# Performance work log

Hardware: AMD Instinct MI355X
Metric: run time of the kernel (lower is better)

## Reference

```python
import jax, jax.numpy as jnp
import numpy as np

H = 32        # num_attention_heads
KVH = 8       # num_key_value_heads
D = 2048      # hidden_size
HD = D // H   # head_dim = 64
GROUPS = H // KVH


def setup_inputs() -> dict:
    key = jax.random.key(0)
    k1, k2, k3, k4 = jax.random.split(key, 4)
    B, T = 2, 2048
    x = jax.random.normal(k1, (B, T, D), dtype=jnp.float32)
    wq = jax.random.normal(k2, (D, H * HD), dtype=jnp.float32) * (D ** -0.5)
    wkv = jax.random.normal(k3, (D, 2 * KVH * HD), dtype=jnp.float32) * (D ** -0.5)
    wo = jax.random.normal(k4, (H * HD, D), dtype=jnp.float32) * (D ** -0.5)
    return {"x": x, "wq": wq, "wkv": wkv, "wo": wo}


def reference(x, wq, wkv, wo):
    B, T, _ = x.shape
    scale = HD ** -0.5
    # projections
    q = (x @ wq).reshape(B, T, H, HD).transpose(0, 2, 1, 3)        # [B,H,T,hd]
    kv = x @ wkv                                                    # [B,T,2*KVH*hd]
    k, v = jnp.split(kv, 2, axis=-1)
    k = k.reshape(B, T, KVH, HD).transpose(0, 2, 1, 3)              # [B,KVH,T,hd]
    v = v.reshape(B, T, KVH, HD).transpose(0, 2, 1, 3)
    # repeat_interleave KV heads to match Q heads
    k = jnp.repeat(k, GROUPS, axis=1)                               # [B,H,T,hd]
    v = jnp.repeat(v, GROUPS, axis=1)
    scores = jnp.einsum('bhqd,bhkd->bhqk', q, k) * scale            # [B,H,T,T]
    causal = jnp.triu(jnp.ones((T, T), dtype=bool), k=1)
    scores = jnp.where(causal, -jnp.inf, scores)
    attn = jax.nn.softmax(scores, axis=-1)
    out = jnp.einsum('bhqk,bhkd->bhqd', attn, v)                    # [B,H,T,hd]
    out = out.transpose(0, 2, 1, 3).reshape(B, T, H * HD)
    return out @ wo
```

## Files before the change

### kernel.cpp

```cpp
#include <hip/hip_runtime.h>

using bf16   = __bf16;
using bf16x8 = __attribute__((ext_vector_type(8))) __bf16;
using f32x4  = __attribute__((ext_vector_type(4))) float;
using u32x4  = __attribute__((ext_vector_type(4))) unsigned;

#define T_SEQ 2048
#define NQKV 3072

__device__ __forceinline__ void async_cp16(const bf16* g, bf16* l) {
  __builtin_amdgcn_global_load_lds((__attribute__((address_space(1))) void*)(void*)g,
                                   (__attribute__((address_space(3))) void*)l, 16, 0, 0);
}

__global__ __launch_bounds__(256) void cvt_kernel(const float* __restrict__ in,
                                                  bf16* __restrict__ out) {
  long i = ((long)blockIdx.x * 256 + threadIdx.x) * 8;
  float4 a = *(const float4*)(in + i);
  float4 c = *(const float4*)(in + i + 4);
  bf16x8 v;
  v[0] = (bf16)a.x; v[1] = (bf16)a.y; v[2] = (bf16)a.z; v[3] = (bf16)a.w;
  v[4] = (bf16)c.x; v[5] = (bf16)c.y; v[6] = (bf16)c.z; v[7] = (bf16)c.w;
  *(bf16x8*)(out + i) = v;
}

__global__ __launch_bounds__(256) void transpose_cvt(const float* __restrict__ in,
                                                     bf16* __restrict__ out,
                                                     int R, int C) {
  __shared__ float tile[32][33];
  const int tc = blockIdx.x * 32;
  const int tr = blockIdx.y * 32;
  const int t = threadIdx.x;
  const int lr = t >> 5;
  const int lc = t & 31;
#pragma unroll
  for (int i = 0; i < 4; ++i)
    tile[lr + i * 8][lc] = in[(size_t)(tr + lr + i * 8) * C + tc + lc];
  __syncthreads();
#pragma unroll
  for (int i = 0; i < 4; ++i)
    out[(size_t)(tc + lr + i * 8) * R + tr + lc] = (bf16)tile[lc][lr + i * 8];
}

__global__ __launch_bounds__(256) void transpose_v(const bf16* __restrict__ in,
                                                   bf16* __restrict__ out) {
  __shared__ bf16 tile[32][33];
  const int c0 = blockIdx.x * 32;
  const int r0 = blockIdx.y * 32;
  const int t = threadIdx.x;
  const int lr = t >> 5;
  const int lc = t & 31;
#pragma unroll
  for (int i = 0; i < 4; ++i)
    tile[lr + i * 8][lc] = in[(size_t)(r0 + lr + i * 8) * NQKV + 2560 + c0 + lc];
  __syncthreads();
#pragma unroll
  for (int i = 0; i < 4; ++i) {
    int c = c0 + lr + i * 8;
    int r = r0 + lc;
    out[(size_t)((r >> 11) * 512 + c) * 2048 + (r & 2047)] = tile[lc][lr + i * 8];
  }
}

template <int KDIM, int BN, bool OUT_BF16>
__global__ __launch_bounds__(512, 2)
void gemm8_kernel(const bf16* __restrict__ A, const bf16* __restrict__ Bt,
                  void* __restrict__ Cout, int Ndim) {
  constexpr int NTILES = KDIM / 64;
  constexpr int NFR = BN / 64;
  __shared__ __attribute__((aligned(16))) bf16 As[2][256 * 64];
  __shared__ __attribute__((aligned(16))) bf16 Bs[2][BN * 64];

  const int tid  = threadIdx.x;
  const int lane = tid & 63;
  const int wave = tid >> 6;
  const int l16  = lane & 15;
  const int q4   = lane >> 4;
  const int wm   = (wave >> 2) * 128;
  const int wn   = (wave & 3) * (BN / 4);

  const long m0 = (long)blockIdx.y * 256;
  const long n0 = (long)blockIdx.x * BN;
  const bf16* Ag = A + m0 * (long)KDIM;
  const bf16* Bg = Bt + n0 * (long)KDIM;

  f32x4 acc[8][NFR] = {};

  auto stage = [&](int buf, int kt) {
    const long k0 = (long)kt * 64;
#pragma unroll
    for (int rr = 0; rr < 4; ++rr) {
      int ci = rr * 512 + tid;
      int row = ci >> 3;
      int ch = (ci & 7) ^ (row & 7);
      async_cp16(Ag + (long)row * KDIM + k0 + ch * 8, &As[buf][ci * 8]);
    }
#pragma unroll
    for (int rr = 0; rr < BN / 64; ++rr) {
      int ci = rr * 512 + tid;
      int row = ci >> 3;
      int ch = (ci & 7) ^ (row & 7);
      async_cp16(Bg + (long)row * KDIM + k0 + ch * 8, &Bs[buf][ci * 8]);
    }
  };

  stage(0, 0);
  stage(1, 1);

  for (int t = 0; t < NTILES; ++t) {
    const int cur = t & 1;
    if (t < NTILES - 1) {
      if constexpr (BN == 256) asm volatile("s_waitcnt vmcnt(8)" ::: "memory");
      else                     asm volatile("s_waitcnt vmcnt(6)" ::: "memory");
    } else {
      asm volatile("s_waitcnt vmcnt(0)" ::: "memory");
    }
    __builtin_amdgcn_s_barrier();

    bf16x8 a0[4], b0[NFR];
#pragma unroll
    for (int mt = 0; mt < 4; ++mt) {
      int row = wm + mt * 16 + l16;
      int slot = q4 ^ (row & 7);
      a0[mt] = *(const bf16x8*)&As[cur][row * 64 + slot * 8];
    }
#pragma unroll
    for (int nt = 0; nt < NFR; ++nt) {
      int row = wn + nt * 16 + l16;
      int slot = q4 ^ (row & 7);
      b0[nt] = *(const bf16x8*)&Bs[cur][row * 64 + slot * 8];
    }
    __builtin_amdgcn_s_setprio(1);
#pragma unroll
    for (int mt = 0; mt < 4; ++mt)
#pragma unroll
      for (int nt = 0; nt < NFR; ++nt)
        acc[mt][nt] = __builtin_amdgcn_mfma_f32_16x16x32_bf16(a0[mt], b0[nt],
                                                              acc[mt][nt], 0, 0, 0);
    __builtin_amdgcn_s_setprio(0);
    bf16x8 a0h[4];
#pragma unroll
    for (int mt = 0; mt < 4; ++mt) {
      int row = wm + 64 + mt * 16 + l16;
      int slot = q4 ^ (row & 7);
      a0h[mt] = *(const bf16x8*)&As[cur][row * 64 + slot * 8];
    }
    __builtin_amdgcn_s_setprio(1);
#pragma unroll
    for (int mt = 0; mt < 4; ++mt)
#pragma unroll
      for (int nt = 0; nt < NFR; ++nt)
        acc[4 + mt][nt] = __builtin_amdgcn_mfma_f32_16x16x32_bf16(a0h[mt], b0[nt],
                                                                  acc[4 + mt][nt], 0, 0, 0);
    __builtin_amdgcn_s_setprio(0);

    bf16x8 a1[4], a1h[4], b1[NFR];
#pragma unroll
    for (int mt = 0; mt < 4; ++mt) {
      int row = wm + mt * 16 + l16;
      int slot = (4 + q4) ^ (row & 7);
      a1[mt] = *(const bf16x8*)&As[cur][row * 64 + slot * 8];
    }
#pragma unroll
    for (int mt = 0; mt < 4; ++mt) {
      int row = wm + 64 + mt * 16 + l16;
      int slot = (4 + q4) ^ (row & 7);
      a1h[mt] = *(const bf16x8*)&As[cur][row * 64 + slot * 8];
    }
#pragma unroll
    for (int nt = 0; nt < NFR; ++nt) {
      int row = wn + nt * 16 + l16;
      int slot = (4 + q4) ^ (row & 7);
      b1[nt] = *(const bf16x8*)&Bs[cur][row * 64 + slot * 8];
    }
    asm volatile("s_waitcnt lgkmcnt(0)" ::: "memory");
    __builtin_amdgcn_sched_barrier(0);
    __builtin_amdgcn_s_barrier();
    if (t + 2 < NTILES) stage(cur, t + 2);

    __builtin_amdgcn_s_setprio(1);
#pragma unroll
    for (int mt = 0; mt < 4; ++mt)
#pragma unroll
      for (int nt = 0; nt < NFR; ++nt)
        acc[mt][nt] = __builtin_amdgcn_mfma_f32_16x16x32_bf16(a1[mt], b1[nt],
                                                              acc[mt][nt], 0, 0, 0);
#pragma unroll
    for (int mt = 0; mt < 4; ++mt)
#pragma unroll
      for (int nt = 0; nt < NFR; ++nt)
        acc[4 + mt][nt] = __builtin_amdgcn_mfma_f32_16x16x32_bf16(a1h[mt], b1[nt],
                                                                  acc[4 + mt][nt], 0, 0, 0);
    __builtin_amdgcn_s_setprio(0);
  }

#pragma unroll
  for (int mt = 0; mt < 8; ++mt)
#pragma unroll
    for (int nt = 0; nt < NFR; ++nt)
#pragma unroll
      for (int r = 0; r < 4; ++r) {
        long row = m0 + wm + mt * 16 + q4 * 4 + r;
        long col = n0 + wn + nt * 16 + l16;
        float v = acc[mt][nt][r];
        if constexpr (OUT_BF16)
          ((bf16*)Cout)[row * Ndim + col] = (bf16)v;
        else
          ((float*)Cout)[row * Ndim + col] = v;
      }
}

__global__ __launch_bounds__(256, 3)
void attn_kernel(const bf16* __restrict__ qkv, const bf16* __restrict__ vT,
                 bf16* __restrict__ outb) {
  __shared__ __attribute__((aligned(16))) bf16 Ks[64 * 64];
  __shared__ __attribute__((aligned(16))) bf16 Vs[64 * 64];

  const int tid  = threadIdx.x;
  const int lane = tid & 63;
  const int wave = tid >> 6;
  const int l16  = lane & 15;
  const int q4   = lane >> 4;

  const int bid = blockIdx.x;
  const int qt  = 15 - (bid >> 6);
  const int bh  = bid & 63;
  const int b   = bh >> 5;
  const int h   = bh & 31;
  const int kvh = h >> 2;
  const long rowbase = (long)b * T_SEQ;

  const int qrow0 = qt * 128;
  const int wq0   = qrow0 + wave * 32;
  const float cexp = 0.125f * 1.4426950408889634f;

  bf16x8 aq[2][2];
#pragma unroll
  for (int mt = 0; mt < 2; ++mt)
#pragma unroll
    for (int ks = 0; ks < 2; ++ks) {
      bf16x8 v = *(const bf16x8*)(qkv +
          (rowbase + wq0 + mt * 16 + l16) * (long)NQKV + h * 64 + ks * 32 + q4 * 8);
#pragma unroll
      for (int i = 0; i < 8; ++i) v[i] = (bf16)((float)v[i] * cexp);
      aq[mt][ks] = v;
    }

  bf16x8 ones_f;
#pragma unroll
  for (int i = 0; i < 8; ++i) ones_f[i] = (l16 == 0) ? (bf16)1.0f : (bf16)0.0f;

  f32x4 o[2][4] = {};
  f32x4 o_l[2] = {};

  const bf16* kbase = qkv + rowbase * (long)NQKV + 2048 + kvh * 64;
  const bf16* vbase = vT + ((long)b * 512 + kvh * 64) * 2048;

  for (int j0 = 0; j0 < qrow0 + 128; j0 += 64) {
    __syncthreads();
    {
#pragma unroll
      for (int h2 = 0; h2 < 2; ++h2) {
        int ci  = h2 * 256 + tid;
        int row = ci >> 3;
        int ch  = (ci & 7) ^ (row & 7);
        *(bf16x8*)&Ks[ci * 8] =
            *(const bf16x8*)(kbase + (long)(j0 + row) * NQKV + ch * 8);
        *(bf16x8*)&Vs[ci * 8] =
            *(const bf16x8*)(vbase + (long)row * 2048 + j0 + ch * 8);
      }
    }
    __syncthreads();
    if (j0 > wq0 + 31) continue;

    f32x4 s[2][4] = {};
#pragma unroll
    for (int ks = 0; ks < 2; ++ks) {
      bf16x8 bk[4];
#pragma unroll
      for (int nt = 0; nt < 4; ++nt) {
        int row  = nt * 16 + l16;
        int slot = (ks * 4 + q4) ^ (row & 7);
        bk[nt] = *(const bf16x8*)&Ks[row * 64 + slot * 8];
      }
#pragma unroll
      for (int mt = 0; mt < 2; ++mt)
#pragma unroll
        for (int nt = 0; nt < 4; ++nt)
          s[mt][nt] = __builtin_amdgcn_mfma_f32_16x16x32_bf16(bk[nt], aq[mt][ks],
                                                              s[mt][nt], 0, 0, 0);
    }

    if (j0 + 63 > wq0) {
#pragma unroll
      for (int mt = 0; mt < 2; ++mt)
#pragma unroll
        for (int nt = 0; nt < 4; ++nt)
#pragma unroll
          for (int r = 0; r < 4; ++r) {
            int rg = wq0 + mt * 16 + l16;
            int cg = j0 + nt * 16 + q4 * 4 + r;
            if (cg > rg) s[mt][nt][r] = -__builtin_inff();
          }
    }

    bf16x8 ap[2][2];
#pragma unroll
    for (int mt = 0; mt < 2; ++mt) {
      unsigned pk0, pk1, pk2, pk3, pk4, pk5, pk6, pk7;
      {
        float p0 = __builtin_amdgcn_exp2f(s[mt][0][0]);
        float p1 = __builtin_amdgcn_exp2f(s[mt][0][1]);
        float p2 = __builtin_amdgcn_exp2f(s[mt][0][2]);
        float p3 = __builtin_amdgcn_exp2f(s[mt][0][3]);
        asm("v_cvt_pk_bf16_f32 %0, %1, %2" : "=v"(pk0) : "v"(p0), "v"(p1));
        asm("v_cvt_pk_bf16_f32 %0, %1, %2" : "=v"(pk1) : "v"(p2), "v"(p3));
      }
      {
        float p0 = __builtin_amdgcn_exp2f(s[mt][1][0]);
        float p1 = __builtin_amdgcn_exp2f(s[mt][1][1]);
        float p2 = __builtin_amdgcn_exp2f(s[mt][1][2]);
        float p3 = __builtin_amdgcn_exp2f(s[mt][1][3]);
        asm("v_cvt_pk_bf16_f32 %0, %1, %2" : "=v"(pk2) : "v"(p0), "v"(p1));
        asm("v_cvt_pk_bf16_f32 %0, %1, %2" : "=v"(pk3) : "v"(p2), "v"(p3));
      }
      {
        float p0 = __builtin_amdgcn_exp2f(s[mt][2][0]);
        float p1 = __builtin_amdgcn_exp2f(s[mt][2][1]);
        float p2 = __builtin_amdgcn_exp2f(s[mt][2][2]);
        float p3 = __builtin_amdgcn_exp2f(s[mt][2][3]);
        asm("v_cvt_pk_bf16_f32 %0, %1, %2" : "=v"(pk4) : "v"(p0), "v"(p1));
        asm("v_cvt_pk_bf16_f32 %0, %1, %2" : "=v"(pk5) : "v"(p2), "v"(p3));
      }
      {
        float p0 = __builtin_amdgcn_exp2f(s[mt][3][0]);
        float p1 = __builtin_amdgcn_exp2f(s[mt][3][1]);
        float p2 = __builtin_amdgcn_exp2f(s[mt][3][2]);
        float p3 = __builtin_amdgcn_exp2f(s[mt][3][3]);
        asm("v_cvt_pk_bf16_f32 %0, %1, %2" : "=v"(pk6) : "v"(p0), "v"(p1));
        asm("v_cvt_pk_bf16_f32 %0, %1, %2" : "=v"(pk7) : "v"(p2), "v"(p3));
      }
      {
        unsigned a0 = pk0, b0 = pk2;
        asm("v_permlane32_swap_b32 %0, %1" : "+v"(a0), "+v"(b0));
        asm("v_permlane16_swap_b32 %0, %1" : "+v"(a0), "+v"(b0));
        unsigned a1 = pk1, b1 = pk3;
        asm("v_permlane32_swap_b32 %0, %1" : "+v"(a1), "+v"(b1));
        asm("v_permlane16_swap_b32 %0, %1" : "+v"(a1), "+v"(b1));
        u32x4 w; w.x = a0; w.y = a1; w.z = b0; w.w = b1;
        ap[mt][0] = __builtin_bit_cast(bf16x8, w);
      }
      {
        unsigned a0 = pk4, b0 = pk6;
        asm("v_permlane32_swap_b32 %0, %1" : "+v"(a0), "+v"(b0));
        asm("v_permlane16_swap_b32 %0, %1" : "+v"(a0), "+v"(b0));
        unsigned a1 = pk5, b1 = pk7;
        asm("v_permlane32_swap_b32 %0, %1" : "+v"(a1), "+v"(b1));
        asm("v_permlane16_swap_b32 %0, %1" : "+v"(a1), "+v"(b1));
        u32x4 w; w.x = a0; w.y = a1; w.z = b0; w.w = b1;
        ap[mt][1] = __builtin_bit_cast(bf16x8, w);
      }
    }

#pragma unroll
    for (int ks = 0; ks < 2; ++ks) {
      bf16x8 bv[4];
#pragma unroll
      for (int dt = 0; dt < 4; ++dt) {
        int row  = dt * 16 + l16;
        int slot = (ks * 4 + q4) ^ (row & 7);
        bv[dt] = *(const bf16x8*)&Vs[row * 64 + slot * 8];
      }
#pragma unroll
      for (int mt = 0; mt < 2; ++mt) {
#pragma unroll
        for (int dt = 0; dt < 4; ++dt)
          o[mt][dt] = __builtin_amdgcn_mfma_f32_16x16x32_bf16(ap[mt][ks], bv[dt],
                                                              o[mt][dt], 0, 0, 0);
        o_l[mt] = __builtin_amdgcn_mfma_f32_16x16x32_bf16(ap[mt][ks], ones_f,
                                                          o_l[mt], 0, 0, 0);
      }
    }
  }

#pragma unroll
  for (int mt = 0; mt < 2; ++mt) {
    float inv[4];
#pragma unroll
    for (int r = 0; r < 4; ++r) {
      float lsum = __shfl(o_l[mt][r], lane & 48);
      inv[r] = 1.0f / lsum;
    }
#pragma unroll
    for (int dt = 0; dt < 4; ++dt)
#pragma unroll
      for (int r = 0; r < 4; ++r) {
        long row = rowbase + wq0 + mt * 16 + q4 * 4 + r;
        int col = h * 64 + dt * 16 + l16;
        outb[row * 2048 + col] = (bf16)(o[mt][dt][r] * inv[r]);
      }
  }
}

extern "C" void kernel_launch(void* const* d_in, const int* in_sizes, int n_in,
                              void* d_out, int out_size, void* d_ws, size_t ws_size,
                              hipStream_t stream) {
  const float* x   = (const float*)d_in[0];
  const float* wq  = (const float*)d_in[1];
  const float* wkv = (const float*)d_in[2];
  const float* wo  = (const float*)d_in[3];
  float* out = (float*)d_out;
  char* ws = (char*)d_ws;

  bf16* xbf  = (bf16*)(ws + 0);
  bf16* w1   = (bf16*)(ws + 16777216);
  bf16* qkv  = (bf16*)(ws + 29360128);
  bf16* attn = xbf;
  bf16* vT   = w1;

  const size_t need_parallel = 54525952u + 8388608u;
  bf16* woT;
  bool woT_early;
  if (ws_size >= need_parallel) {
    woT = (bf16*)(ws + 54525952);
    woT_early = true;
  } else {
    woT = qkv;
    woT_early = false;
  }

  cvt_kernel<<<4096, 256, 0, stream>>>(x, xbf);
  transpose_cvt<<<dim3(64, 64), 256, 0, stream>>>(wq, w1, 2048, 2048);
  transpose_cvt<<<dim3(32, 64), 256, 0, stream>>>(wkv, w1 + 2048L * 2048, 2048, 1024);
  if (woT_early)
    transpose_cvt<<<dim3(64, 64), 256, 0, stream>>>(wo, woT, 2048, 2048);

  gemm8_kernel<2048, 256, true><<<dim3(12, 16), 512, 0, stream>>>(xbf, w1, (void*)qkv, 3072);

  transpose_v<<<dim3(16, 128), 256, 0, stream>>>(qkv, vT);

  attn_kernel<<<1024, 256, 0, stream>>>(qkv, vT, attn);

  if (!woT_early)
    transpose_cvt<<<dim3(64, 64), 256, 0, stream>>>(wo, woT, 2048, 2048);

  gemm8_kernel<2048, 128, false><<<dim3(16, 16), 512, 0, stream>>>(attn, woT, (void*)out, 2048);
}
```

Measured before the change: 260.6 us.

## Interleave GEMM tile loads in halves across four MFMA phases

Rewrites the GEMM main loop into four compute phases, each preceded by fragment loads and a slice of async global-to-LDS staging for the next tile (A halves and B halves spread across phases). The goal is to spread memory traffic evenly and cut register use by reusing a single fragment set, instead of issuing the whole next-tile prefetch in one burst. In exchange it adds several extra workgroup barriers per k-tile and a tighter vmcnt wait, which could stall the MFMA pipeline.

After: 280.8 us. 1.08x slower.

```diff
diff --git a/kernel.cpp b/kernel.cpp
--- a/kernel.cpp
+++ b/kernel.cpp
@@ -64,9 +64,9 @@
 
 template <int KDIM, int BN, bool OUT_BF16>
 __global__ __launch_bounds__(512, 2)
-void gemm8_kernel(const bf16* __restrict__ A, const bf16* __restrict__ Bt,
-                  void* __restrict__ Cout, int Ndim) {
-  constexpr int NTILES = KDIM / 64;
+void gemm8p_kernel(const bf16* __restrict__ A, const bf16* __restrict__ Bt,
+                   void* __restrict__ Cout, int Ndim) {
+  constexpr int NT  = KDIM / 64;
   constexpr int NFR = BN / 64;
   __shared__ __attribute__((aligned(16))) bf16 As[2][256 * 64];
   __shared__ __attribute__((aligned(16))) bf16 Bs[2][BN * 64];
@@ -86,128 +86,145 @@
 
   f32x4 acc[8][NFR] = {};
 
-  auto stage = [&](int buf, int kt) {
+  auto stageA = [&](int buf, int kt, int h) {
     const long k0 = (long)kt * 64;
 #pragma unroll
-    for (int rr = 0; rr < 4; ++rr) {
-      int ci = rr * 512 + tid;
-      int row = ci >> 3;
-      int ch = (ci & 7) ^ (row & 7);
-      async_cp16(Ag + (long)row * KDIM + k0 + ch * 8, &As[buf][ci * 8]);
-    }
-#pragma unroll
-    for (int rr = 0; rr < BN / 64; ++rr) {
-      int ci = rr * 512 + tid;
-      int row = ci >> 3;
-      int ch = (ci & 7) ^ (row & 7);
-      async_cp16(Bg + (long)row * KDIM + k0 + ch * 8, &Bs[buf][ci * 8]);
+    for (int rr = 0; rr < 2; ++rr) {
+      int ci  = rr * 512 + tid;
+      int row = h * 128 + (ci >> 3);
+      int ch  = (ci & 7) ^ (row & 7);
+      async_cp16(Ag + (long)row * KDIM + k0 + ch * 8,
+                 &As[buf][(size_t)row * 64 + (ci & 7) * 8]);
     }
   };
-
-  stage(0, 0);
-  stage(1, 1);
-
-  for (int t = 0; t < NTILES; ++t) {
-    const int cur = t & 1;
-    if (t < NTILES - 1) {
-      if constexpr (BN == 256) asm volatile("s_waitcnt vmcnt(8)" ::: "memory");
-      else                     asm volatile("s_waitcnt vmcnt(6)" ::: "memory");
-    } else {
-      asm volatile("s_waitcnt vmcnt(0)" ::: "memory");
-    }
-    __builtin_amdgcn_s_barrier();
-
-    bf16x8 a0[4], b0[NFR];
+  auto stageB = [&](int buf, int kt, int h) {
+    const long k0 = (long)kt * 64;
+#pragma unroll
+    for (int rr = 0; rr < 2; ++rr) {
+      int ci  = rr * 512 + tid;
+      int row = h * 128 + (ci >> 3);
+      int ch  = (ci & 7) ^ (row & 7);
+      async_cp16(Bg + (long)row * KDIM + k0 + ch * 8,
+                 &Bs[buf][(size_t)row * 64 + (ci & 7) * 8]);
+    }
+  };
+
+  stageA(0, 0, 0);
+  stageA(0, 0, 1);
+  stageB(0, 0, 0);
+  if constexpr (BN == 256) stageB(0, 0, 1);
+  stageB(1, 1, 0);
+
+  bf16x8 aF[4], bF[NFR];
+
+  for (int t = 0; t < NT; ++t) {
+    const int cur = t & 1, nxt = cur ^ 1;
+    if (t < NT - 1) asm volatile("s_waitcnt vmcnt(2)" ::: "memory");
+    else            asm volatile("s_waitcnt vmcnt(0)" ::: "memory");
+    __builtin_amdgcn_s_barrier();
+
 #pragma unroll
     for (int mt = 0; mt < 4; ++mt) {
       int row = wm + mt * 16 + l16;
-      int slot = q4 ^ (row & 7);
-      a0[mt] = *(const bf16x8*)&As[cur][row * 64 + slot * 8];
+      aF[mt] = *(const bf16x8*)&As[cur][row * 64 + (q4 ^ (row & 7)) * 8];
     }
 #pragma unroll
     for (int nt = 0; nt < NFR; ++nt) {
       int row = wn + nt * 16 + l16;
-      int slot = q4 ^ (row & 7);
-      b0[nt] = *(const bf16x8*)&Bs[cur][row * 64 + slot * 8];
-    }
+      bF[nt] = *(const bf16x8*)&Bs[cur][row * 64 + (q4 ^ (row & 7)) * 8];
+    }
+    if constexpr (BN == 256) { if (t + 1 < NT) stageB(nxt, t + 1, 1); }
+    __builtin_amdgcn_s_barrier();
+    asm volatile("s_waitcnt lgkmcnt(0)" ::: "memory");
+    __builtin_amdgcn_sched_barrier(0);
     __builtin_amdgcn_s_setprio(1);
 #pragma unroll
     for (int mt = 0; mt < 4; ++mt)
 #pragma unroll
       for (int nt = 0; nt < NFR; ++nt)
-        acc[mt][nt] = __builtin_amdgcn_mfma_f32_16x16x32_bf16(a0[mt], b0[nt],
+        acc[mt][nt] = __builtin_amdgcn_mfma_f32_16x16x32_bf16(aF[mt], bF[nt],
                                                               acc[mt][nt], 0, 0, 0);
     __builtin_amdgcn_s_setprio(0);
-    bf16x8 a0h[4];
+    __builtin_amdgcn_s_barrier();
+
 #pragma unroll
     for (int mt = 0; mt < 4; ++mt) {
       int row = wm + 64 + mt * 16 + l16;
-      int slot = q4 ^ (row & 7);
-      a0h[mt] = *(const bf16x8*)&As[cur][row * 64 + slot * 8];
-    }
+      aF[mt] = *(const bf16x8*)&As[cur][row * 64 + (q4 ^ (row & 7)) * 8];
+    }
+    if (t + 1 < NT) stageA(nxt, t + 1, 0);
+    __builtin_amdgcn_s_barrier();
+    asm volatile("s_waitcnt lgkmcnt(0)" ::: "memory");
+    __builtin_amdgcn_sched_barrier(0);
     __builtin_amdgcn_s_setprio(1);
 #pragma unroll
     for (int mt = 0; mt < 4; ++mt)
 #pragma unroll
       for (int nt = 0; nt < NFR; ++nt)
-        acc[4 + mt][nt] = __builtin_amdgcn_mfma_f32_16x16x32_bf16(a0h[mt], b0[nt],
+        acc[4 + mt][nt] = __builtin_amdgcn_mfma_f32_16x16x32_bf16(aF[mt], bF[nt],
                                                                   acc[4 + mt][nt], 0, 0, 0);
     __builtin_amdgcn_s_setprio(0);
-
-    bf16x8 a1[4], a1h[4], b1[NFR];
+    __builtin_amdgcn_s_barrier();
+
 #pragma unroll
     for (int mt = 0; mt < 4; ++mt) {
       int row = wm + mt * 16 + l16;
-      int slot = (4 + q4) ^ (row & 7);
-      a1[mt] = *(const bf16x8*)&As[cur][row * 64 + slot * 8];
-    }
+      aF[mt] = *(const bf16x8*)&As[cur][row * 64 + ((4 + q4) ^ (row & 7)) * 8];
+    }
+#pragma unroll
+    for (int nt = 0; nt < NFR; ++nt) {
+      int row = wn + nt * 16 + l16;
+      bF[nt] = *(const bf16x8*)&Bs[cur][row * 64 + ((4 + q4) ^ (row & 7)) * 8];
+    }
+    if (t + 1 < NT) stageA(nxt, t + 1, 1);
+    __builtin_amdgcn_s_barrier();
+    asm volatile("s_waitcnt lgkmcnt(0)" ::: "memory");
+    __builtin_amdgcn_sched_barrier(0);
+    __builtin_amdgcn_s_setprio(1);
+#pragma unroll
+    for (int mt = 0; mt < 4; ++mt)
+#pragma unroll
+      for (int nt = 0; nt < NFR; ++nt)
+        acc[mt][nt] = __builtin_amdgcn_mfma_f32_16x16x32_bf16(aF[mt], bF[nt],
+                                                              acc[mt][nt], 0, 0, 0);
+    __builtin_amdgcn_s_setprio(0);
+    __builtin_amdgcn_s_barrier();
+
 #pragma unroll
     for (int mt = 0; mt < 4; ++mt) {
       int row = wm + 64 + mt * 16 + l16;
-      int slot = (4 + q4) ^ (row & 7);
-      a1h[mt] = *(const bf16x8*)&As[cur][row * 64 + slot * 8];
-    }
-#pragma unroll
-    for (int nt = 0; nt < NFR; ++nt) {
-      int row = wn + nt * 16 + l16;
-      int slot = (4 + q4) ^ (row & 7);
-      b1[nt] = *(const bf16x8*)&Bs[cur][row * 64 + slot * 8];
-    }
+      aF[mt] = *(const bf16x8*)&As[cur][row * 64 + ((4 + q4) ^ (row & 7)) * 8];
+    }
+    if (t + 2 < NT) stageB(cur, t + 2, 0);
+    __builtin_amdgcn_s_barrier();
     asm volatile("s_waitcnt lgkmcnt(0)" ::: "memory");
     __builtin_amdgcn_sched_barrier(0);
-    __builtin_amdgcn_s_barrier();
-    if (t + 2 < NTILES) stage(cur, t + 2);
-
     __builtin_amdgcn_s_setprio(1);
 #pragma unroll
     for (int mt = 0; mt < 4; ++mt)
 #pragma unroll
       for (int nt = 0; nt < NFR; ++nt)
-        acc[mt][nt] = __builtin_amdgcn_mfma_f32_16x16x32_bf16(a1[mt], b1[nt],
-                                                              acc[mt][nt], 0, 0, 0);
-#pragma unroll
-    for (int mt = 0; mt < 4; ++mt)
-#pragma unroll
-      for (int nt = 0; nt < NFR; ++nt)
-        acc[4 + mt][nt] = __builtin_amdgcn_mfma_f32_16x16x32_bf16(a1h[mt], b1[nt],
+        acc[4 + mt][nt] = __builtin_amdgcn_mfma_f32_16x16x32_bf16(aF[mt], bF[nt],
                                                                   acc[4 + mt][nt], 0, 0, 0);
     __builtin_amdgcn_s_setprio(0);
   }
 
 #pragma unroll
-  for (int mt = 0; mt < 8; ++mt)
+  for (int idx = 0; idx < 8; ++idx) {
+    const int mh = idx >> 2, mt = idx & 3;
 #pragma unroll
     for (int nt = 0; nt < NFR; ++nt)
 #pragma unroll
       for (int r = 0; r < 4; ++r) {
-        long row = m0 + wm + mt * 16 + q4 * 4 + r;
+        long row = m0 + wm + mh * 64 + mt * 16 + q4 * 4 + r;
         long col = n0 + wn + nt * 16 + l16;
-        float v = acc[mt][nt][r];
+        float v = acc[idx][nt][r];
         if constexpr (OUT_BF16)
           ((bf16*)Cout)[row * Ndim + col] = (bf16)v;
         else
           ((float*)Cout)[row * Ndim + col] = v;
       }
+  }
 }
 
 __global__ __launch_bounds__(256, 3)
@@ -435,7 +452,7 @@
   if (woT_early)
     transpose_cvt<<<dim3(64, 64), 256, 0, stream>>>(wo, woT, 2048, 2048);
 
-  gemm8_kernel<2048, 256, true><<<dim3(12, 16), 512, 0, stream>>>(xbf, w1, (void*)qkv, 3072);
+  gemm8p_kernel<2048, 256, true><<<dim3(12, 16), 512, 0, stream>>>(xbf, w1, (void*)qkv, 3072);
 
   transpose_v<<<dim3(16, 128), 256, 0, stream>>>(qkv, vT);
 
@@ -444,5 +461,5 @@
   if (!woT_early)
     transpose_cvt<<<dim3(64, 64), 256, 0, stream>>>(wo, woT, 2048, 2048);
 
-  gemm8_kernel<2048, 128, false><<<dim3(16, 16), 512, 0, stream>>>(attn, woT, (void*)out, 2048);
-}
+  gemm8p_kernel<2048, 128, false><<<dim3(16, 16), 512, 0, stream>>>(attn, woT, (void*)out, 2048);
+}
```
